# Optimization experiments

Hardware: AMD Instinct MI355X
Metric: run time of the kernel (lower is better)

Reference implementation:

```python
import math
import jax, jax.numpy as jnp
import numpy as np

B, T, C, H = 4, 2048, 1024, 16
D = C // H  # head dim = 64


def setup_inputs() -> dict:
    key = jax.random.key(0)
    ks = jax.random.split(key, 9)
    s = 1.0 / math.sqrt(C)
    return {
        "x": jax.random.normal(ks[0], (B, T, C), jnp.float32),
        "Wq": jax.random.normal(ks[1], (C, C), jnp.float32) * s,
        "bq": jax.random.normal(ks[2], (C,), jnp.float32) * 0.02,
        "Wk": jax.random.normal(ks[3], (C, C), jnp.float32) * s,
        "bk": jax.random.normal(ks[4], (C,), jnp.float32) * 0.02,
        "Wv": jax.random.normal(ks[5], (C, C), jnp.float32) * s,
        "bv": jax.random.normal(ks[6], (C,), jnp.float32) * 0.02,
        "Wo": jax.random.normal(ks[7], (C, C), jnp.float32) * s,
        "bo": jax.random.normal(ks[8], (C,), jnp.float32) * 0.02,
    }


def reference(x, Wq, bq, Wk, bk, Wv, bv, Wo, bo):
    # Projections: (B,T,C) -> (B,H,T,D)
    def heads(y):
        return y.reshape(B, T, H, D).transpose(0, 2, 1, 3)

    q = heads(x @ Wq + bq)
    k = heads(x @ Wk + bk)
    v = heads(x @ Wv + bv)

    scale = 1.0 / math.sqrt(D)
    scores = jnp.einsum("bhqd,bhkd->bhqk", q, k) * scale  # (B,H,T,T)
    causal = jnp.tril(jnp.ones((T, T), dtype=bool))
    scores = jnp.where(causal[None, None], scores, jnp.float32(-jnp.inf))
    att = jax.nn.softmax(scores, axis=-1)

    y = jnp.einsum("bhqk,bhkd->bhqd", att, v)  # (B,H,T,D)
    y = y.transpose(0, 2, 1, 3).reshape(B, T, C)
    return y @ Wo + bo
```

## Files before the change

kernel.cpp:

```cpp
#include <hip/hip_runtime.h>

#define B_ 4
#define T_ 2048
#define C_ 1024
#define H_ 16
#define D_ 64
#define M_ (B_*T_)
#define CR3 3072

typedef unsigned short u16;
typedef __attribute__((ext_vector_type(8))) short short8;
typedef __attribute__((ext_vector_type(8))) unsigned short ushort8_t;
typedef __attribute__((ext_vector_type(4))) unsigned short ushort4_t;
typedef __attribute__((ext_vector_type(4))) float floatx4;
typedef __attribute__((ext_vector_type(16))) float f32x16;
typedef __attribute__((ext_vector_type(4))) unsigned int uint4_t;

__device__ __forceinline__ u16 f2bf(float f) {
  union { float f; unsigned u; } v; v.f = f;
  unsigned r = v.u + 0x7fffu + ((v.u >> 16) & 1u);
  return (u16)(r >> 16);
}

__device__ __forceinline__ void gload16(const void* g, void* l) {
  __builtin_amdgcn_global_load_lds((__attribute__((address_space(1))) void*)(g),
                                   (__attribute__((address_space(3))) void*)(l),
                                   16, 0, 0);
}

__device__ __forceinline__ unsigned cvtpk(float lo, float hi) {
  unsigned r;
  asm("v_cvt_pk_bf16_f32 %0, %1, %2" : "=v"(r) : "v"(lo), "v"(hi));
  return r;
}

__device__ __forceinline__ void pl32swap(unsigned &a, unsigned &b) {
  asm volatile("v_permlane32_swap_b32 %0, %1" : "+v"(a), "+v"(b));
}

#define MFMA32(a, b, c) __builtin_amdgcn_mfma_f32_32x32x16_bf16(a, b, c, 0, 0, 0)

__global__ __launch_bounds__(256) void convx_k(const float* __restrict__ x,
                                               u16* __restrict__ o) {
  int i = (blockIdx.x * 256 + threadIdx.x) * 4;
  floatx4 v = *(const floatx4*)(x + i);
  ushort4_t r;
#pragma unroll
  for (int j = 0; j < 4; ++j) r[j] = f2bf(v[j]);
  *(ushort4_t*)(o + i) = r;
}

__global__ __launch_bounds__(256) void wconv_k(const float* __restrict__ W0,
                                               const float* __restrict__ W1,
                                               const float* __restrict__ W2,
                                               const float* __restrict__ W3,
                                               u16* __restrict__ WT) {
  __shared__ float tile[64][65];
  const float* W = blockIdx.z == 0 ? W0 : blockIdx.z == 1 ? W1 : blockIdx.z == 2 ? W2 : W3;
  const float sc = blockIdx.z == 0 ? 0.125f * 1.44269504f : 1.0f;
  u16* Wt = WT + (size_t)blockIdx.z * (C_ * C_);
  int k0 = blockIdx.x * 64, n0 = blockIdx.y * 64;
  int t = threadIdx.x;
  int r = t >> 2, c0 = (t & 3) * 16;
#pragma unroll
  for (int j = 0; j < 4; ++j) {
    floatx4 v = *(const floatx4*)(W + (size_t)(k0 + r) * C_ + n0 + c0 + j * 4);
#pragma unroll
    for (int jj = 0; jj < 4; ++jj) tile[r][c0 + j * 4 + jj] = v[jj];
  }
  __syncthreads();
  ushort8_t o0, o1;
#pragma unroll
  for (int j = 0; j < 8; ++j) o0[j] = f2bf(tile[c0 + j][r] * sc);
#pragma unroll
  for (int j = 0; j < 8; ++j) o1[j] = f2bf(tile[c0 + 8 + j][r] * sc);
  *(ushort8_t*)(Wt + (size_t)(n0 + r) * C_ + k0 + c0) = o0;
  *(ushort8_t*)(Wt + (size_t)(n0 + r) * C_ + k0 + c0 + 8) = o1;
}

template <int OUTF32>
__global__ __launch_bounds__(256, 2) void gemm_k(const u16* __restrict__ A,
                                                 const u16* __restrict__ Wt,
                                                 const float* __restrict__ b0,
                                                 const float* __restrict__ b1,
                                                 const float* __restrict__ b2,
                                                 float bsc0,
                                                 void* __restrict__ Cout, int ostride) {
  __shared__ u16 As[128 * 32];
  __shared__ u16 Bs[128 * 32];
  const int tid = threadIdx.x;
  const int w = tid >> 6, lane = tid & 63;
  const int wr = (w >> 1) * 64, wc = (w & 1) * 64;
  const int l15 = lane & 15, g = lane >> 4;
  const int m0 = blockIdx.x * 128, n0 = blockIdx.y * 128;

  floatx4 acc[4][4] = {};

  const u16* ga = A + (size_t)(m0 + (tid >> 2)) * C_ + (tid & 3) * 8;
  const u16* gb = Wt + (size_t)(n0 + (tid >> 2)) * C_ + (tid & 3) * 8;
  u16* lA = As + tid * 8;
  u16* lB = Bs + tid * 8;

  for (int kt = 0; kt < C_; kt += 32) {
    gload16(ga + kt, lA);
    gload16(ga + kt + (size_t)64 * C_, lA + 64 * 32);
    gload16(gb + kt, lB);
    gload16(gb + kt + (size_t)64 * C_, lB + 64 * 32);
    asm volatile("s_waitcnt vmcnt(0)" ::: "memory");
    __syncthreads();
    short8 af[4], bf[4];
#pragma unroll
    for (int i = 0; i < 4; ++i)
      af[i] = *(const short8*)(As + (wr + i * 16 + l15) * 32 + g * 8);
#pragma unroll
    for (int i = 0; i < 4; ++i)
      bf[i] = *(const short8*)(Bs + (wc + i * 16 + l15) * 32 + g * 8);
#pragma unroll
    for (int mi = 0; mi < 4; ++mi)
#pragma unroll
      for (int ni = 0; ni < 4; ++ni)
        acc[mi][ni] = __builtin_amdgcn_mfma_f32_16x16x32_bf16(af[mi], bf[ni], acc[mi][ni], 0, 0, 0);
    __syncthreads();
  }
#pragma unroll
  for (int mi = 0; mi < 4; ++mi) {
    int row = m0 + wr + mi * 16 + g * 4;
#pragma unroll
    for (int ni = 0; ni < 4; ++ni) {
      int col = n0 + wc + ni * 16 + l15;
      int seg = col >> 10;
      const float* bp = seg == 0 ? b0 : seg == 1 ? b1 : b2;
      float bv = bp[col & 1023] * (seg == 0 ? bsc0 : 1.0f);
#pragma unroll
      for (int i = 0; i < 4; ++i) {
        float v = acc[mi][ni][i] + bv;
        if (OUTF32)
          ((float*)Cout)[(size_t)(row + i) * ostride + col] = v;
        else
          ((u16*)Cout)[(size_t)(row + i) * ostride + col] = f2bf(v);
      }
    }
  }
}

__global__ __launch_bounds__(256, 2) void attn_k(const u16* __restrict__ QKV,
                                                 u16* __restrict__ Yg) {
  __shared__ u16 Ks[2][64 * 64];
  __shared__ u16 Vt[2][64 * 64];

  const int tid = threadIdx.x;
  const int w = tid >> 6, lane = tid & 63;
  const int qi = lane & 31, h = lane >> 5;

  const int lid = blockIdx.x;
  const int a4 = lid >> 6;
  const int gq = a4 >> 2, iq = a4 & 3;
  const int jt = gq == 0 ? 15 - 2 * iq : gq == 1 ? 2 * iq : gq == 2 ? 14 - 2 * iq : 1 + 2 * iq;
  const int bh = lid & 63;
  const int nt = 2 * jt + 2;

  const size_t baseQ = (size_t)(bh >> 4) * T_ * CR3 + (size_t)(bh & 15) * D_;
  const size_t baseY = (size_t)(bh >> 4) * T_ * C_ + (size_t)(bh & 15) * D_;
  const u16* Kg = QKV + baseQ + 1024;
  const u16* Vg = QKV + baseQ + 2048;

  const int srow = tid >> 3, schunk = tid & 7;
  const int sgcol = (schunk ^ (srow & 7)) * 8;
  const u16* Kgr = Kg + (size_t)srow * CR3 + sgcol;
  const u16* Vgr = Vg + (size_t)srow * CR3 + schunk * 8;

  const int qw0 = 128 * jt + 32 * w;
  const int q_abs = qw0 + qi;

  short8 qf0, qf1, qf2, qf3;
  {
    const u16* Qr = QKV + baseQ + (size_t)q_abs * CR3 + 8 * h;
    qf0 = *(const short8*)(Qr);      qf1 = *(const short8*)(Qr + 16);
    qf2 = *(const short8*)(Qr + 32); qf3 = *(const short8*)(Qr + 48);
  }

  ushort8_t va, vbr;
  gload16(Kgr, &Ks[0][tid * 8]);
  gload16(Kgr + (size_t)32 * CR3, &Ks[0][2048 + tid * 8]);
  va = *(const ushort8_t*)(Vgr);
  vbr = *(const ushort8_t*)(Vgr + (size_t)32 * CR3);

  f32x16 y0 = {}, y1 = {};
  float l_run = 0.f;
  const float M0 = 13.0f;

  for (int t = 0; t < nt; ++t) {
    const int kv0 = t * 64;
    u16* Kb = Ks[t & 1];
    u16* Vb = Vt[t & 1];
    asm volatile("s_waitcnt vmcnt(0)" ::: "memory");
    {
      char* vbp = (char*)Vb;
#pragma unroll
      for (int j = 0; j < 8; ++j) {
        int d = schunk * 8 + j;
        int sl = ((schunk ^ j) & 7) << 4;
        *(u16*)(vbp + d * 128 + ((2 * srow) ^ sl)) = va[j];
        *(u16*)(vbp + d * 128 + ((2 * (srow + 32)) ^ sl)) = vbr[j];
      }
    }
    __syncthreads();
    if (t + 1 < nt) {
      int nkv = (t + 1) * 64;
      u16* dst = Ks[(t + 1) & 1];
      gload16(Kgr + (size_t)nkv * CR3, dst + tid * 8);
      gload16(Kgr + (size_t)(nkv + 32) * CR3, dst + 2048 + tid * 8);
      va = *(const ushort8_t*)(Vgr + (size_t)nkv * CR3);
      vbr = *(const ushort8_t*)(Vgr + (size_t)(nkv + 32) * CR3);
    }

    if (kv0 <= qw0 + 31) {
      f32x16 s0 = {}, s1 = {};
      {
        const int swq = (qi & 7) << 4;
        const char* kr0 = (const char*)Kb + qi * 128;
        const char* kr1 = (const char*)Kb + (qi + 32) * 128;
        short8 k0, k1;
        k0 = *(const short8*)(kr0 + ((16 * h) ^ swq));
        k1 = *(const short8*)(kr1 + ((16 * h) ^ swq));
        s0 = MFMA32(k0, qf0, s0); s1 = MFMA32(k1, qf0, s1);
        k0 = *(const short8*)(kr0 + ((32 + 16 * h) ^ swq));
        k1 = *(const short8*)(kr1 + ((32 + 16 * h) ^ swq));
        s0 = MFMA32(k0, qf1, s0); s1 = MFMA32(k1, qf1, s1);
        k0 = *(const short8*)(kr0 + ((64 + 16 * h) ^ swq));
        k1 = *(const short8*)(kr1 + ((64 + 16 * h) ^ swq));
        s0 = MFMA32(k0, qf2, s0); s1 = MFMA32(k1, qf2, s1);
        k0 = *(const short8*)(kr0 + ((96 + 16 * h) ^ swq));
        k1 = *(const short8*)(kr1 + ((96 + 16 * h) ^ swq));
        s0 = MFMA32(k0, qf3, s0); s1 = MFMA32(k1, qf3, s1);
      }
      if (kv0 + 63 > qw0) {
#pragma unroll
        for (int r = 0; r < 16; ++r) {
          int kvq = (r & 3) + 8 * (r >> 2) + 4 * h;
          if (kv0 + kvq > q_abs) s0[r] = -1e30f;
          if (kv0 + 32 + kvq > q_abs) s1[r] = -1e30f;
        }
      }
#pragma unroll
      for (int r = 0; r < 16; ++r) s0[r] = __builtin_amdgcn_exp2f(s0[r] - M0);
#pragma unroll
      for (int r = 0; r < 16; ++r) s1[r] = __builtin_amdgcn_exp2f(s1[r] - M0);
      {
        float a8[8];
#pragma unroll
        for (int r = 0; r < 8; ++r) a8[r] = (s0[r] + s0[r + 8]) + (s1[r] + s1[r + 8]);
#pragma unroll
        for (int r = 0; r < 4; ++r) a8[r] += a8[r + 4];
        l_run += (a8[0] + a8[1]) + (a8[2] + a8[3]);
      }
      unsigned pw[16];
      {
        unsigned a0, b0, a1, b1;
        a0 = cvtpk(s0[0], s0[1]);  b0 = cvtpk(s0[4], s0[5]);  pl32swap(a0, b0);
        a1 = cvtpk(s0[2], s0[3]);  b1 = cvtpk(s0[6], s0[7]);  pl32swap(a1, b1);
        pw[0] = a0; pw[1] = a1; pw[2] = b0; pw[3] = b1;
        a0 = cvtpk(s0[8], s0[9]);  b0 = cvtpk(s0[12], s0[13]); pl32swap(a0, b0);
        a1 = cvtpk(s0[10], s0[11]); b1 = cvtpk(s0[14], s0[15]); pl32swap(a1, b1);
        pw[4] = a0; pw[5] = a1; pw[6] = b0; pw[7] = b1;
        a0 = cvtpk(s1[0], s1[1]);  b0 = cvtpk(s1[4], s1[5]);  pl32swap(a0, b0);
        a1 = cvtpk(s1[2], s1[3]);  b1 = cvtpk(s1[6], s1[7]);  pl32swap(a1, b1);
        pw[8] = a0; pw[9] = a1; pw[10] = b0; pw[11] = b1;
        a0 = cvtpk(s1[8], s1[9]);  b0 = cvtpk(s1[12], s1[13]); pl32swap(a0, b0);
        a1 = cvtpk(s1[10], s1[11]); b1 = cvtpk(s1[14], s1[15]); pl32swap(a1, b1);
        pw[12] = a0; pw[13] = a1; pw[14] = b0; pw[15] = b1;
      }
      {
        const char* vb0 = (const char*)Vb + qi * 128;
        const char* vb1 = (const char*)Vb + (qi + 32) * 128;
        const int sx0 = (((qi >> 3) ^ qi) & 7) << 4;
        const int sx1 = sx0 ^ 0x40;
#pragma unroll
        for (int c = 0; c < 4; ++c) {
          int cb = 32 * c + 16 * h;
          uint4_t pt = {pw[c * 4 + 0], pw[c * 4 + 1], pw[c * 4 + 2], pw[c * 4 + 3]};
          short8 pa = __builtin_bit_cast(short8, pt);
          short8 v0 = *(const short8*)(vb0 + (cb ^ sx0));
          short8 v1 = *(const short8*)(vb1 + (cb ^ sx1));
          y0 = MFMA32(pa, v0, y0);
          y1 = MFMA32(pa, v1, y1);
        }
      }
    }
    __syncthreads();
  }

  l_run += __shfl_xor(l_run, 32);
  float linv = 1.0f / l_run;
#pragma unroll
  for (int r = 0; r < 16; ++r) {
    int qp = (r & 3) + 8 * (r >> 2) + 4 * h;
    float lv = __shfl(linv, qp);
    size_t row = baseY + (size_t)(qw0 + qp) * C_;
    Yg[row + qi] = f2bf(y0[r] * lv);
    Yg[row + 32 + qi] = f2bf(y1[r] * lv);
  }
}

extern "C" void kernel_launch(void* const* d_in, const int* in_sizes, int n_in,
                              void* d_out, int out_size, void* d_ws, size_t ws_size,
                              hipStream_t stream) {
  const float* x  = (const float*)d_in[0];
  const float* Wq = (const float*)d_in[1];
  const float* bq = (const float*)d_in[2];
  const float* Wk = (const float*)d_in[3];
  const float* bk = (const float*)d_in[4];
  const float* Wv = (const float*)d_in[5];
  const float* bv = (const float*)d_in[6];
  const float* Wo = (const float*)d_in[7];
  const float* bo = (const float*)d_in[8];
  float* out = (float*)d_out;

  char* ws = (char*)d_ws;
  u16* xb   = (u16*)ws;
  u16* WT   = (u16*)(ws + (size_t)16777216);
  u16* QKVb = (u16*)(ws + (size_t)25165824);
  u16* Yb = xb;

  convx_k<<<dim3(M_ * C_ / 1024), 256, 0, stream>>>(x, xb);
  wconv_k<<<dim3(16, 16, 4), 256, 0, stream>>>(Wq, Wk, Wv, Wo, WT);
  gemm_k<0><<<dim3(64, 24), 256, 0, stream>>>(xb, WT, bq, bk, bv, 0.125f * 1.44269504f,
                                              QKVb, CR3);
  attn_k<<<dim3(1024), 256, 0, stream>>>(QKVb, Yb);
  gemm_k<1><<<dim3(64, 8), 256, 0, stream>>>(Yb, WT + (size_t)3 * 1048576, bo, bo, bo, 1.0f,
                                             out, C_);
}
```

Baseline: 170.0 us.

## Add 256x256-tile double-buffered QKV GEMM with swizzled LDS and XCD-aware block mapping

Replaces the 128x128 single-buffered QKV projection GEMM with a new 512-thread kernel that computes 256x256 output tiles, uses K=64 steps, and double-buffers LDS with async global-to-LDS loads that overlap the next stage with compute. LDS rows are XOR-swizzled to avoid bank conflicts, and block IDs are remapped across the 8 XCDs for better L2 locality. The aim is higher arithmetic intensity and less exposed load latency. In exchange it uses 128 KB of LDS per block, which limits occupancy, and it adds more register pressure. The output-projection GEMM gets a simplified bias path.

```diff
diff --git a/kernel.cpp b/kernel.cpp
--- a/kernel.cpp
+++ b/kernel.cpp
@@ -39,6 +39,7 @@
 }
 
 #define MFMA32(a, b, c) __builtin_amdgcn_mfma_f32_32x32x16_bf16(a, b, c, 0, 0, 0)
+#define MFMA16(a, b, c) __builtin_amdgcn_mfma_f32_16x16x32_bf16(a, b, c, 0, 0, 0)
 
 __global__ __launch_bounds__(256) void convx_k(const float* __restrict__ x,
                                                u16* __restrict__ o) {
@@ -78,13 +79,107 @@
   *(ushort8_t*)(Wt + (size_t)(n0 + r) * C_ + k0 + c0 + 8) = o1;
 }
 
+__global__ __launch_bounds__(512, 2) void gemm8_k(const u16* __restrict__ A,
+                                                  const u16* __restrict__ Wt,
+                                                  const float* __restrict__ b0,
+                                                  const float* __restrict__ b1,
+                                                  const float* __restrict__ b2,
+                                                  float bsc0,
+                                                  u16* __restrict__ Cout) {
+  __shared__ u16 lds[65536];
+  const int tid = threadIdx.x;
+  const int lane = tid & 63, w = tid >> 6;
+  const int wm = w >> 2, wn = w & 3;
+  const int l15 = lane & 15, g = lane >> 4;
+  const int swl = (l15 & 7) << 3;
+
+  const int nwg = gridDim.x, cpx = nwg >> 3, bid = blockIdx.x;
+  const int swz = (bid & 7) * cpx + (bid >> 3);
+  const int bm = swz & 31, bn = swz >> 5;
+  const int m0 = bm * 256, n0 = bn * 256;
+
+  const int srow = tid >> 3;
+  const int scol = ((tid & 7) ^ (srow & 7)) * 8;
+  const u16* gA = A + (size_t)(m0 + srow) * 1024 + scol;
+  const u16* gB = Wt + (size_t)(n0 + srow) * 1024 + scol;
+
+#define STAGE8(KT, BUF) do { \
+    u16* la_ = lds + (BUF) * 32768 + tid * 8; \
+    const u16* pa_ = gA + (KT) * 64; \
+    const u16* pb_ = gB + (KT) * 64; \
+    gload16(pa_, la_);                 gload16(pa_ + 64 * 1024, la_ + 4096); \
+    gload16(pa_ + 128 * 1024, la_ + 8192); gload16(pa_ + 192 * 1024, la_ + 12288); \
+    gload16(pb_, la_ + 16384);         gload16(pb_ + 64 * 1024, la_ + 20480); \
+    gload16(pb_ + 128 * 1024, la_ + 24576); gload16(pb_ + 192 * 1024, la_ + 28672); \
+  } while (0)
+
+  floatx4 acc[8][4] = {};
+
+  STAGE8(0, 0);
+  STAGE8(1, 1);
+  asm volatile("s_waitcnt vmcnt(8)" ::: "memory");
+  __syncthreads();
+
+  for (int t = 0; t < 16; ++t) {
+    const u16* Ab = lds + (t & 1) * 32768;
+    const u16* Bb = Ab + 16384;
+    short8 bfr[4][2];
+#pragma unroll
+    for (int ni = 0; ni < 4; ++ni)
+#pragma unroll
+      for (int ks = 0; ks < 2; ++ks)
+        bfr[ni][ks] = *(const short8*)(Bb + (wn * 64 + ni * 16 + l15) * 64 +
+                                       ((ks * 32 + g * 8) ^ swl));
+#pragma unroll
+    for (int mh = 0; mh < 2; ++mh) {
+      short8 af[4][2];
+#pragma unroll
+      for (int mi = 0; mi < 4; ++mi)
+#pragma unroll
+        for (int ks = 0; ks < 2; ++ks)
+          af[mi][ks] = *(const short8*)(Ab + (wm * 128 + mh * 64 + mi * 16 + l15) * 64 +
+                                        ((ks * 32 + g * 8) ^ swl));
+      __builtin_amdgcn_s_setprio(1);
+#pragma unroll
+      for (int mi = 0; mi < 4; ++mi)
+#pragma unroll
+        for (int ni = 0; ni < 4; ++ni)
+#pragma unroll
+          for (int ks = 0; ks < 2; ++ks)
+            acc[mh * 4 + mi][ni] = MFMA16(af[mi][ks], bfr[ni][ks], acc[mh * 4 + mi][ni]);
+      __builtin_amdgcn_s_setprio(0);
+    }
+    __syncthreads();
+    if (t + 2 < 16) {
+      STAGE8(t + 2, t & 1);
+      asm volatile("s_waitcnt vmcnt(8)" ::: "memory");
+      __syncthreads();
+    } else if (t == 14) {
+      asm volatile("s_waitcnt vmcnt(0)" ::: "memory");
+      __syncthreads();
+    }
+  }
+
+#pragma unroll
+  for (int mi8 = 0; mi8 < 8; ++mi8) {
+    int row = m0 + wm * 128 + (mi8 >> 2) * 64 + (mi8 & 3) * 16 + g * 4;
+#pragma unroll
+    for (int ni = 0; ni < 4; ++ni) {
+      int col = n0 + wn * 64 + ni * 16 + l15;
+      int seg = col >> 10;
+      const float* bp = seg == 0 ? b0 : seg == 1 ? b1 : b2;
+      float bv = bp[col & 1023] * (seg == 0 ? bsc0 : 1.0f);
+#pragma unroll
+      for (int i = 0; i < 4; ++i)
+        Cout[(size_t)(row + i) * CR3 + col] = f2bf(acc[mi8][ni][i] + bv);
+    }
+  }
+}
+
 template <int OUTF32>
 __global__ __launch_bounds__(256, 2) void gemm_k(const u16* __restrict__ A,
                                                  const u16* __restrict__ Wt,
                                                  const float* __restrict__ b0,
-                                                 const float* __restrict__ b1,
-                                                 const float* __restrict__ b2,
-                                                 float bsc0,
                                                  void* __restrict__ Cout, int ostride) {
   __shared__ u16 As[128 * 32];
   __shared__ u16 Bs[128 * 32];
@@ -119,7 +214,7 @@
     for (int mi = 0; mi < 4; ++mi)
 #pragma unroll
       for (int ni = 0; ni < 4; ++ni)
-        acc[mi][ni] = __builtin_amdgcn_mfma_f32_16x16x32_bf16(af[mi], bf[ni], acc[mi][ni], 0, 0, 0);
+        acc[mi][ni] = MFMA16(af[mi], bf[ni], acc[mi][ni]);
     __syncthreads();
   }
 #pragma unroll
@@ -128,9 +223,7 @@
 #pragma unroll
     for (int ni = 0; ni < 4; ++ni) {
       int col = n0 + wc + ni * 16 + l15;
-      int seg = col >> 10;
-      const float* bp = seg == 0 ? b0 : seg == 1 ? b1 : b2;
-      float bv = bp[col & 1023] * (seg == 0 ? bsc0 : 1.0f);
+      float bv = b0[col];
 #pragma unroll
       for (int i = 0; i < 4; ++i) {
         float v = acc[mi][ni][i] + bv;
@@ -324,9 +417,7 @@
 
   convx_k<<<dim3(M_ * C_ / 1024), 256, 0, stream>>>(x, xb);
   wconv_k<<<dim3(16, 16, 4), 256, 0, stream>>>(Wq, Wk, Wv, Wo, WT);
-  gemm_k<0><<<dim3(64, 24), 256, 0, stream>>>(xb, WT, bq, bk, bv, 0.125f * 1.44269504f,
-                                              QKVb, CR3);
+  gemm8_k<<<dim3(384), 512, 0, stream>>>(xb, WT, bq, bk, bv, 0.125f * 1.44269504f, QKVb);
   attn_k<<<dim3(1024), 256, 0, stream>>>(QKVb, Yb);
-  gemm_k<1><<<dim3(64, 8), 256, 0, stream>>>(Yb, WT + (size_t)3 * 1048576, bo, bo, bo, 1.0f,
-                                             out, C_);
-}
+  gemm_k<1><<<dim3(64, 8), 256, 0, stream>>>(Yb, WT + (size_t)3 * 1048576, bo, out, C_);
+}
```

Result: slower. 188.1 us (+10.7%).

## Add pipelined 128x256 QKV GEMM with XOR-swizzled LDS and block swizzle

Applied to the files above, without the earlier changes.

Replaces the QKV projection GEMM with a new 512-thread kernel using 128x256 tiles, a 4-deep LDS ring with async global-to-LDS loads issued two stages ahead, and partial vmcnt waits so loads overlap MFMA work. LDS rows are XOR-swizzled in both GEMMs to cut bank conflicts. Block indices are remapped for L2 locality, and s_setprio raises wave priority around the MFMA block. The output GEMM is simplified to a single bias pointer. The new kernel uses more LDS (96KB) and registers, which may limit occupancy.

```diff
diff --git a/kernel.cpp b/kernel.cpp
--- a/kernel.cpp
+++ b/kernel.cpp
@@ -39,6 +39,7 @@
 }
 
 #define MFMA32(a, b, c) __builtin_amdgcn_mfma_f32_32x32x16_bf16(a, b, c, 0, 0, 0)
+#define MFMA16(a, b, c) __builtin_amdgcn_mfma_f32_16x16x32_bf16(a, b, c, 0, 0, 0)
 
 __global__ __launch_bounds__(256) void convx_k(const float* __restrict__ x,
                                                u16* __restrict__ o) {
@@ -78,13 +79,91 @@
   *(ushort8_t*)(Wt + (size_t)(n0 + r) * C_ + k0 + c0 + 8) = o1;
 }
 
+__global__ __launch_bounds__(512, 2) void gemm8_k(const u16* __restrict__ A,
+                                                  const u16* __restrict__ Wt,
+                                                  const float* __restrict__ b0,
+                                                  const float* __restrict__ b1,
+                                                  const float* __restrict__ b2,
+                                                  float bsc0,
+                                                  u16* __restrict__ Cout) {
+  __shared__ u16 lds4[49152];
+  const int tid = threadIdx.x;
+  const int lane = tid & 63, w = tid >> 6;
+  const int wm = w >> 2, wn = w & 3;
+  const int l15 = lane & 15, g = lane >> 4;
+
+  const int bid = blockIdx.x;
+  const int swz = (bid & 7) * 96 + (bid >> 3);
+  const int bm = swz & 63, bn = swz >> 6;
+  const int m0 = bm * 128, n0 = bn * 256;
+
+  const int srow = tid >> 2;
+  const int scol = ((tid & 3) ^ ((srow >> 1) & 3)) * 8;
+  const u16* gA  = A  + (size_t)(m0 + srow) * 1024 + scol;
+  const u16* gB1 = Wt + (size_t)(n0 + srow) * 1024 + scol;
+  const u16* gB2 = Wt + (size_t)(n0 + 128 + srow) * 1024 + scol;
+
+#define STAGE(KT) do { \
+    u16* s_ = lds4 + ((KT) & 3) * 12288; \
+    gload16(gA  + (KT) * 32, s_ + tid * 8); \
+    gload16(gB1 + (KT) * 32, s_ + 4096 + tid * 8); \
+    gload16(gB2 + (KT) * 32, s_ + 8192 + tid * 8); \
+  } while (0)
+
+  floatx4 acc[4][4] = {};
+
+  STAGE(0);
+  STAGE(1);
+
+  for (int kt = 0; kt < 32; ++kt) {
+    if (kt < 30) STAGE(kt + 2);
+    if (kt < 30)       asm volatile("s_waitcnt vmcnt(6)" ::: "memory");
+    else if (kt == 30) asm volatile("s_waitcnt vmcnt(3)" ::: "memory");
+    else               asm volatile("s_waitcnt vmcnt(0)" ::: "memory");
+    __builtin_amdgcn_s_barrier();
+
+    const u16* Ab = lds4 + (kt & 3) * 12288;
+    const u16* Bb = Ab + 4096;
+    short8 af[4], bf[4];
+#pragma unroll
+    for (int mi = 0; mi < 4; ++mi) {
+      int ra = wm * 64 + mi * 16 + l15;
+      af[mi] = *(const short8*)(Ab + ra * 32 + ((g ^ ((ra >> 1) & 3)) << 3));
+    }
+#pragma unroll
+    for (int ni = 0; ni < 4; ++ni) {
+      int rb = wn * 64 + ni * 16 + l15;
+      bf[ni] = *(const short8*)(Bb + rb * 32 + ((g ^ ((rb >> 1) & 3)) << 3));
+    }
+    __builtin_amdgcn_s_setprio(1);
+#pragma unroll
+    for (int mi = 0; mi < 4; ++mi)
+#pragma unroll
+      for (int ni = 0; ni < 4; ++ni)
+        acc[mi][ni] = MFMA16(af[mi], bf[ni], acc[mi][ni]);
+    __builtin_amdgcn_s_setprio(0);
+  }
+
+#pragma unroll
+  for (int mi = 0; mi < 4; ++mi) {
+    int row = m0 + wm * 64 + mi * 16 + g * 4;
+#pragma unroll
+    for (int ni = 0; ni < 4; ++ni) {
+      int col = n0 + wn * 64 + ni * 16 + l15;
+      int seg = col >> 10;
+      const float* bp = seg == 0 ? b0 : seg == 1 ? b1 : b2;
+      float bv = bp[col & 1023] * (seg == 0 ? bsc0 : 1.0f);
+#pragma unroll
+      for (int i = 0; i < 4; ++i)
+        Cout[(size_t)(row + i) * CR3 + col] = f2bf(acc[mi][ni][i] + bv);
+    }
+  }
+}
+
 template <int OUTF32>
 __global__ __launch_bounds__(256, 2) void gemm_k(const u16* __restrict__ A,
                                                  const u16* __restrict__ Wt,
                                                  const float* __restrict__ b0,
-                                                 const float* __restrict__ b1,
-                                                 const float* __restrict__ b2,
-                                                 float bsc0,
                                                  void* __restrict__ Cout, int ostride) {
   __shared__ u16 As[128 * 32];
   __shared__ u16 Bs[128 * 32];
@@ -96,8 +175,10 @@
 
   floatx4 acc[4][4] = {};
 
-  const u16* ga = A + (size_t)(m0 + (tid >> 2)) * C_ + (tid & 3) * 8;
-  const u16* gb = Wt + (size_t)(n0 + (tid >> 2)) * C_ + (tid & 3) * 8;
+  const int srow = tid >> 2;
+  const int scol = ((tid & 3) ^ ((srow >> 1) & 3)) * 8;
+  const u16* ga = A + (size_t)(m0 + srow) * C_ + scol;
+  const u16* gb = Wt + (size_t)(n0 + srow) * C_ + scol;
   u16* lA = As + tid * 8;
   u16* lB = Bs + tid * 8;
 
@@ -110,16 +191,20 @@
     __syncthreads();
     short8 af[4], bf[4];
 #pragma unroll
-    for (int i = 0; i < 4; ++i)
-      af[i] = *(const short8*)(As + (wr + i * 16 + l15) * 32 + g * 8);
-#pragma unroll
-    for (int i = 0; i < 4; ++i)
-      bf[i] = *(const short8*)(Bs + (wc + i * 16 + l15) * 32 + g * 8);
+    for (int i = 0; i < 4; ++i) {
+      int ra = wr + i * 16 + l15;
+      af[i] = *(const short8*)(As + ra * 32 + ((g ^ ((ra >> 1) & 3)) << 3));
+    }
+#pragma unroll
+    for (int i = 0; i < 4; ++i) {
+      int rb = wc + i * 16 + l15;
+      bf[i] = *(const short8*)(Bs + rb * 32 + ((g ^ ((rb >> 1) & 3)) << 3));
+    }
 #pragma unroll
     for (int mi = 0; mi < 4; ++mi)
 #pragma unroll
       for (int ni = 0; ni < 4; ++ni)
-        acc[mi][ni] = __builtin_amdgcn_mfma_f32_16x16x32_bf16(af[mi], bf[ni], acc[mi][ni], 0, 0, 0);
+        acc[mi][ni] = MFMA16(af[mi], bf[ni], acc[mi][ni]);
     __syncthreads();
   }
 #pragma unroll
@@ -128,9 +213,7 @@
 #pragma unroll
     for (int ni = 0; ni < 4; ++ni) {
       int col = n0 + wc + ni * 16 + l15;
-      int seg = col >> 10;
-      const float* bp = seg == 0 ? b0 : seg == 1 ? b1 : b2;
-      float bv = bp[col & 1023] * (seg == 0 ? bsc0 : 1.0f);
+      float bv = b0[col];
 #pragma unroll
       for (int i = 0; i < 4; ++i) {
         float v = acc[mi][ni][i] + bv;
@@ -324,9 +407,7 @@
 
   convx_k<<<dim3(M_ * C_ / 1024), 256, 0, stream>>>(x, xb);
   wconv_k<<<dim3(16, 16, 4), 256, 0, stream>>>(Wq, Wk, Wv, Wo, WT);
-  gemm_k<0><<<dim3(64, 24), 256, 0, stream>>>(xb, WT, bq, bk, bv, 0.125f * 1.44269504f,
-                                              QKVb, CR3);
+  gemm8_k<<<dim3(768), 512, 0, stream>>>(xb, WT, bq, bk, bv, 0.125f * 1.44269504f, QKVb);
   attn_k<<<dim3(1024), 256, 0, stream>>>(QKVb, Yb);
-  gemm_k<1><<<dim3(64, 8), 256, 0, stream>>>(Yb, WT + (size_t)3 * 1048576, bo, bo, bo, 1.0f,
-                                             out, C_);
-}
+  gemm_k<1><<<dim3(64, 8), 256, 0, stream>>>(Yb, WT + (size_t)3 * 1048576, bo, out, C_);
+}
```

Result: faster. 165.3 us (-2.8%).
